# Kernel tuning notes

Hardware: AMD Instinct MI355X
Metric: run time of the kernel (lower is better)

## Reference

```python
import jax, jax.numpy as jnp
import numpy as np

B, T, N, D = 4, 16, 1024, 128
LN_EPS = 1e-5


def setup_inputs() -> dict:
    key = jax.random.key(0)
    k1, k2, k3 = jax.random.split(key, 3)
    X = jax.random.normal(k1, (B, T, N, D), dtype=jnp.float32)
    # normalized adjacency (dense, values in [0,1))
    A = jax.random.uniform(k2, (N, N), dtype=jnp.float32)
    # GCN linear weight (torch nn.Linear, bias=False): out = x @ W.T
    W = jax.random.normal(k3, (D, D), dtype=jnp.float32) / np.sqrt(D)
    gamma = jnp.ones((D,), dtype=jnp.float32)
    beta = jnp.zeros((D,), dtype=jnp.float32)
    return {"X": X, "A": A, "W": W, "gamma": gamma, "beta": beta}


def reference(X, A, W, gamma, beta):
    d = X.shape[-1]
    inv_sqrt_d_a = np.float32(1.0 / np.sqrt(d + 1e-8))  # score scale
    inv_sqrt_d_b = np.float32(1.0 / np.sqrt(d + 1e-9))  # output scale
    # dynamic attention-like scores over nodes: (b,T,N,N)
    scores = jnp.einsum('btnd,btmd->btnm', X, X)
    St = jax.nn.softmax(scores, axis=-1) * inv_sqrt_d_a  # dropout p=0 => identity
    Aeff = A * St                                        # adjacency-masked attention
    # GCN: relu((Aeff @ X) @ W.T)
    h = jnp.einsum('btnm,btmd->btnd', Aeff, X)
    h = jax.nn.relu(h @ W.T) * inv_sqrt_d_b
    # LayerNorm over last dim
    mu = jnp.mean(h, axis=-1, keepdims=True)
    var = jnp.mean(jnp.square(h - mu), axis=-1, keepdims=True)
    h = (h - mu) * jax.lax.rsqrt(var + LN_EPS) * gamma + beta
    # residual
    return h + X
```

## Files before the change

### kernel.cpp

```cpp
#include <hip/hip_runtime.h>


#define NNODES 1024
#define DDIM   128
#define BROWS  128
#define WROWS  16
#define MC     64
#define NCHUNK (NNODES / MC)
#define THREADS 512

#define CA 0.08838834764831845f
#define CB 0.08838834764831845f
#define LN_EPS 1e-5f

typedef __attribute__((ext_vector_type(8))) short bf16x8;
typedef __attribute__((ext_vector_type(4))) float f32x4;

#define XBF_S 136
#define XBT_S 72
#define P_S   72
#define H_S   136
#define XBF_OFF 0
#define XBT_OFF 8704
#define P_OFF   17920
#define SM_TOT  27136

__device__ __forceinline__ unsigned short f2bf(float f) {
  unsigned int u = __float_as_uint(f);
  u += 0x7FFFu + ((u >> 16) & 1u);
  return (unsigned short)(u >> 16);
}

__device__ __forceinline__ bf16x8 pack8(float4 a, float4 b) {
  union { bf16x8 v; unsigned short u[8]; } pk;
  pk.u[0] = f2bf(a.x); pk.u[1] = f2bf(a.y); pk.u[2] = f2bf(a.z); pk.u[3] = f2bf(a.w);
  pk.u[4] = f2bf(b.x); pk.u[5] = f2bf(b.y); pk.u[6] = f2bf(b.z); pk.u[7] = f2bf(b.w);
  return pk.v;
}

__global__ __launch_bounds__(THREADS, 4)
void sdgcn_fused(const float* __restrict__ X, const float* __restrict__ A,
                 const float* __restrict__ W, const float* __restrict__ gamma,
                 const float* __restrict__ beta, float* __restrict__ Out) {
  const int bt   = blockIdx.x;
  const int row0 = blockIdx.y * BROWS;
  const int tid  = (int)threadIdx.x;
  const int wid  = tid >> 6;
  const int lane = tid & 63;
  const int c    = lane & 15;
  const int q    = lane >> 4;

  const float* Xbt = X + (size_t)bt * NNODES * DDIM;

  __shared__ __align__(16) unsigned short sm[SM_TOT];
  unsigned short* Pw = sm + P_OFF + wid * (WROWS * P_S);

  const int wswz = 16 * (q >> 1);
  const int rswz = 16 * ((c >> 3) & 1);

  bf16x8 qfrag[4];
  float cn[4];
  {
    const float* qrow = Xbt + (size_t)(row0 + wid * WROWS + c) * DDIM;
    float ss = 0.f;
#pragma unroll
    for (int ds = 0; ds < 4; ++ds) {
      const float* p = qrow + ds * 32 + q * 8;
      float4 a = *(const float4*)p;
      float4 b = *(const float4*)(p + 4);
      ss += a.x*a.x + a.y*a.y + a.z*a.z + a.w*a.w;
      ss += b.x*b.x + b.y*b.y + b.z*b.z + b.w*b.w;
      qfrag[ds] = pack8(a, b);
    }
    ss += __shfl_xor(ss, 16, 64);
    ss += __shfl_xor(ss, 32, 64);
#pragma unroll
    for (int r = 0; r < 4; ++r)
      cn[r] = __shfl(ss, (lane & 48) + ((lane & 48) >> 2) + r, 64);
  }

  float z_st[4] = {0.f, 0.f, 0.f, 0.f};
  f32x4 Ofr[8];
#pragma unroll
  for (int dt = 0; dt < 8; ++dt) Ofr[dt] = (f32x4){0.f, 0.f, 0.f, 0.f};

  const int grow = row0 + wid * WROWS + q * 4;

  const int sm_ = tid >> 5, sd4 = tid & 31;
  float4 stg[4];
#pragma unroll
  for (int k = 0; k < 4; ++k)
    stg[k] = *(const float4*)(Xbt + (size_t)(sm_ + k * 16) * DDIM + sd4 * 4);

  for (int ch = 0; ch < NCHUNK; ++ch) {
    const int m0 = ch * MC;
#pragma unroll
    for (int k = 0; k < 4; ++k) {
      float4 v = stg[k];
      unsigned int lo = (unsigned int)f2bf(v.x) | ((unsigned int)f2bf(v.y) << 16);
      unsigned int hi = (unsigned int)f2bf(v.z) | ((unsigned int)f2bf(v.w) << 16);
      *(uint2*)(sm + XBF_OFF + (sm_ + k * 16) * XBF_S + sd4 * 4) = make_uint2(lo, hi);
    }
    __syncthreads();
    if (ch + 1 < NCHUNK) {
      const float* nx = Xbt + (size_t)(m0 + MC) * DDIM;
#pragma unroll
      for (int k = 0; k < 4; ++k)
        stg[k] = *(const float4*)(nx + (size_t)(sm_ + k * 16) * DDIM + sd4 * 4);
    }
    float av[4][4];
#pragma unroll
    for (int r = 0; r < 4; ++r)
#pragma unroll
      for (int mt = 0; mt < 4; ++mt)
        av[r][mt] = A[(size_t)(grow + r) * NNODES + m0 + mt*16 + c];
#pragma unroll
    for (int k = 0; k < 2; ++k) {
      int task = tid + k * THREADS;
      int d = task & 127, m8 = task >> 7;
      int base = XBF_OFF + d;
      unsigned int w0 = (unsigned int)sm[base + (m8*8+0)*XBF_S] | ((unsigned int)sm[base + (m8*8+1)*XBF_S] << 16);
      unsigned int w1 = (unsigned int)sm[base + (m8*8+2)*XBF_S] | ((unsigned int)sm[base + (m8*8+3)*XBF_S] << 16);
      unsigned int w2 = (unsigned int)sm[base + (m8*8+4)*XBF_S] | ((unsigned int)sm[base + (m8*8+5)*XBF_S] << 16);
      unsigned int w3 = (unsigned int)sm[base + (m8*8+6)*XBF_S] | ((unsigned int)sm[base + (m8*8+7)*XBF_S] << 16);
      *(uint4*)(sm + XBT_OFF + d * XBT_S + m8 * 8) = make_uint4(w0, w1, w2, w3);
    }
    f32x4 S[4];
#pragma unroll
    for (int mt = 0; mt < 4; ++mt) {
      f32x4 acc = (f32x4){0.f, 0.f, 0.f, 0.f};
#pragma unroll
      for (int ds = 0; ds < 4; ++ds) {
        bf16x8 bf = *(const bf16x8*)(sm + XBF_OFF + (mt*16 + c) * XBF_S + ds*32 + q*8);
        acc = __builtin_amdgcn_mfma_f32_16x16x32_bf16(qfrag[ds], bf, acc, 0, 0, 0);
      }
      S[mt] = acc;
    }
    __syncthreads();
#pragma unroll
    for (int r = 0; r < 4; ++r) {
      float zr = 0.f;
#pragma unroll
      for (int mt = 0; mt < 4; ++mt) {
        float p = __expf(S[mt][r] - cn[r]);
        zr += p;
        Pw[(q*4 + r) * P_S + (((mt*16) ^ wswz) + c)] = f2bf(p * av[r][mt]);
      }
      z_st[r] += zr;
    }
#pragma unroll
    for (int ks = 0; ks < 2; ++ks) {
      bf16x8 pf = *(const bf16x8*)(Pw + c * P_S + (((ks*32 + q*8) ^ rswz)));
#pragma unroll
      for (int dt = 0; dt < 8; ++dt) {
        bf16x8 vf = *(const bf16x8*)(sm + XBT_OFF + (dt*16 + c) * XBT_S + ks*32 + q*8);
        Ofr[dt] = __builtin_amdgcn_mfma_f32_16x16x32_bf16(pf, vf, Ofr[dt], 0, 0, 0);
      }
    }
  }

#pragma unroll
  for (int r = 0; r < 4; ++r) {
    float z = z_st[r];
#pragma unroll
    for (int off = 1; off < 16; off <<= 1) z += __shfl_xor(z, off, 64);
    z_st[r] = z;
  }

  __syncthreads();
  unsigned short* Hw = sm + XBT_OFF + wid * (WROWS * H_S);
#pragma unroll
  for (int r = 0; r < 4; ++r) {
    float rinv = CA / z_st[r];
#pragma unroll
    for (int dt = 0; dt < 8; ++dt)
      Hw[(q*4 + r) * H_S + (((dt*16) ^ wswz) + c)] = f2bf(Ofr[dt][r] * rinv);
  }
  f32x4 G[8];
#pragma unroll
  for (int jt = 0; jt < 8; ++jt) G[jt] = (f32x4){0.f, 0.f, 0.f, 0.f};
#pragma unroll
  for (int ks = 0; ks < 4; ++ks) {
    bf16x8 hf = *(const bf16x8*)(Hw + c * H_S + (((ks*32 + q*8) ^ rswz)));
#pragma unroll
    for (int jt = 0; jt < 8; ++jt) {
      const float* wr = W + (size_t)(jt*16 + c) * DDIM + ks*32 + q*8;
      float4 a = *(const float4*)wr;
      float4 b = *(const float4*)(wr + 4);
      bf16x8 wf = pack8(a, b);
      G[jt] = __builtin_amdgcn_mfma_f32_16x16x32_bf16(hf, wf, G[jt], 0, 0, 0);
    }
  }
#pragma unroll
  for (int jt = 0; jt < 8; ++jt) {
#pragma unroll
    for (int r = 0; r < 4; ++r) G[jt][r] = fmaxf(G[jt][r], 0.f) * CB;
  }
  float* Obt = Out + (size_t)bt * NNODES * DDIM;
#pragma unroll
  for (int r = 0; r < 4; ++r) {
    float s1 = 0.f, s2 = 0.f;
#pragma unroll
    for (int jt = 0; jt < 8; ++jt) { float v = G[jt][r]; s1 += v; s2 += v * v; }
#pragma unroll
    for (int off = 1; off < 16; off <<= 1) {
      s1 += __shfl_xor(s1, off, 64);
      s2 += __shfl_xor(s2, off, 64);
    }
    float mu = s1 * (1.f / 128.f);
    float va = s2 * (1.f / 128.f) - mu * mu;
    float rs = rsqrtf(va + LN_EPS);
    const float* xr = Xbt + (size_t)(grow + r) * DDIM;
    float* orow = Obt + (size_t)(grow + r) * DDIM;
#pragma unroll
    for (int jt = 0; jt < 8; ++jt) {
      int col = jt * 16 + c;
      orow[col] = (G[jt][r] - mu) * rs * gamma[col] + beta[col] + xr[col];
    }
  }
}

extern "C" void kernel_launch(void* const* d_in, const int* in_sizes, int n_in,
                              void* d_out, int out_size, void* d_ws, size_t ws_size,
                              hipStream_t stream) {
  const float* X     = (const float*)d_in[0];
  const float* A     = (const float*)d_in[1];
  const float* W     = (const float*)d_in[2];
  const float* gamma = (const float*)d_in[3];
  const float* beta  = (const float*)d_in[4];
  float* Out = (float*)d_out;
  dim3 grid(64, NNODES / BROWS);
  hipLaunchKernelGGL(sdgcn_fused, grid, dim3(THREADS), 0, stream, X, A, W, gamma, beta, Out);
}
```

Before: 181.4 us.

## Add bf16 prepass that writes X, X-transpose and W to workspace

Adds a prepass kernel that converts X to bf16 in both row-major and transposed layouts, and W to bf16, storing them in the workspace. The main kernel then reads the bf16 keys straight from global/L2 for the score MFMAs, double-buffers the transposed X tiles in shared memory, and loads W already in bf16. This removes the per-chunk fp32-to-bf16 conversion and the LDS transpose that each of the 8 row blocks per batch repeated. In exchange it adds a second launch plus extra workspace writes and reads, and the score B-operand now comes from global memory instead of LDS. The old fused kernel is kept as a fallback when the workspace is too small.

```diff
diff --git a/kernel.cpp b/kernel.cpp
--- a/kernel.cpp
+++ b/kernel.cpp
@@ -3,11 +3,8 @@
 
 #define NNODES 1024
 #define DDIM   128
-#define BROWS  128
-#define WROWS  16
 #define MC     64
 #define NCHUNK (NNODES / MC)
-#define THREADS 512
 
 #define CA 0.08838834764831845f
 #define CB 0.08838834764831845f
@@ -15,6 +12,233 @@
 
 typedef __attribute__((ext_vector_type(8))) short bf16x8;
 typedef __attribute__((ext_vector_type(4))) float f32x4;
+typedef unsigned short ushort_t;
+
+__device__ __forceinline__ unsigned short f2bf(float f) {
+  unsigned int u = __float_as_uint(f);
+  u += 0x7FFFu + ((u >> 16) & 1u);
+  return (unsigned short)(u >> 16);
+}
+__device__ __forceinline__ float bf2f(unsigned short u) {
+  return __uint_as_float(((unsigned int)u) << 16);
+}
+
+__global__ __launch_bounds__(256, 8)
+void sdgcn_prepass(const float* __restrict__ X, const float* __restrict__ W,
+                   ushort_t* __restrict__ Xr, ushort_t* __restrict__ XT,
+                   ushort_t* __restrict__ Wb) {
+  const int bt = blockIdx.x, mt = blockIdx.y, m0 = mt * 64;
+  const int tid = (int)threadIdx.x;
+  __shared__ __align__(16) ushort_t sm[17920];
+  const float* Xs = X + ((size_t)bt * NNODES + m0) * DDIM;
+  ushort_t* Xro = Xr + ((size_t)bt * NNODES + m0) * DDIM;
+#pragma unroll
+  for (int k = 0; k < 8; ++k) {
+    int idx = tid + k * 256;
+    int m = idx >> 5, d4 = idx & 31;
+    float4 v = *(const float4*)(Xs + (size_t)m * DDIM + d4 * 4);
+    unsigned int lo = (unsigned int)f2bf(v.x) | ((unsigned int)f2bf(v.y) << 16);
+    unsigned int hi = (unsigned int)f2bf(v.z) | ((unsigned int)f2bf(v.w) << 16);
+    *(uint2*)(sm + m * 136 + d4 * 4) = make_uint2(lo, hi);
+    *(uint2*)(Xro + (size_t)m * DDIM + d4 * 4) = make_uint2(lo, hi);
+  }
+  __syncthreads();
+#pragma unroll
+  for (int k = 0; k < 4; ++k) {
+    int task = tid + k * 256;
+    int d = task & 127, m8 = task >> 7;
+    int base = d;
+    unsigned int w0 = (unsigned int)sm[base + (m8*8+0)*136] | ((unsigned int)sm[base + (m8*8+1)*136] << 16);
+    unsigned int w1 = (unsigned int)sm[base + (m8*8+2)*136] | ((unsigned int)sm[base + (m8*8+3)*136] << 16);
+    unsigned int w2 = (unsigned int)sm[base + (m8*8+4)*136] | ((unsigned int)sm[base + (m8*8+5)*136] << 16);
+    unsigned int w3 = (unsigned int)sm[base + (m8*8+6)*136] | ((unsigned int)sm[base + (m8*8+7)*136] << 16);
+    *(uint4*)(sm + 8704 + d * 72 + m8 * 8) = make_uint4(w0, w1, w2, w3);
+  }
+  __syncthreads();
+#pragma unroll
+  for (int k = 0; k < 4; ++k) {
+    int task = tid + k * 256;
+    int d = task >> 3, seg = task & 7;
+    uint4 w = *(const uint4*)(sm + 8704 + d * 72 + seg * 8);
+    *(uint4*)(XT + ((size_t)bt * DDIM + d) * NNODES + m0 + seg * 8) = w;
+  }
+  if (bt == 0 && mt < 4) {
+    const float* ws = W + mt * 4096 + tid * 16;
+    ushort_t* wd = Wb + mt * 4096 + tid * 16;
+#pragma unroll
+    for (int k = 0; k < 4; ++k) {
+      float4 v = *(const float4*)(ws + k * 4);
+      unsigned int lo = (unsigned int)f2bf(v.x) | ((unsigned int)f2bf(v.y) << 16);
+      unsigned int hi = (unsigned int)f2bf(v.z) | ((unsigned int)f2bf(v.w) << 16);
+      *(uint2*)(wd + k * 4) = make_uint2(lo, hi);
+    }
+  }
+}
+
+__global__ __launch_bounds__(512, 4)
+void sdgcn_main(const float* __restrict__ X, const float* __restrict__ A,
+                const float* __restrict__ gamma, const float* __restrict__ beta,
+                const ushort_t* __restrict__ Xr, const ushort_t* __restrict__ XT,
+                const ushort_t* __restrict__ Wb, float* __restrict__ Out) {
+  const int bt   = blockIdx.x;
+  const int row0 = blockIdx.y * 128;
+  const int tid  = (int)threadIdx.x;
+  const int wid  = tid >> 6;
+  const int lane = tid & 63;
+  const int c    = lane & 15;
+  const int q    = lane >> 4;
+
+  const ushort_t* Xrb = Xr + (size_t)bt * NNODES * DDIM;
+  const ushort_t* XTb = XT + (size_t)bt * DDIM * NNODES;
+
+  __shared__ __align__(16) ushort_t sm[27648];
+  ushort_t* Pw = sm + 18432 + wid * 1152;
+
+  const int wswz = 16 * (q >> 1);
+  const int rswz = 16 * ((c >> 3) & 1);
+
+  bf16x8 qfrag[4];
+  float cn[4];
+  {
+    const ushort_t* qrow = Xrb + (size_t)(row0 + wid * 16 + c) * DDIM;
+    float ss = 0.f;
+#pragma unroll
+    for (int ds = 0; ds < 4; ++ds) {
+      qfrag[ds] = *(const bf16x8*)(qrow + ds * 32 + q * 8);
+      union { bf16x8 v; unsigned short u[8]; } t; t.v = qfrag[ds];
+#pragma unroll
+      for (int j = 0; j < 8; ++j) { float v = bf2f(t.u[j]); ss += v * v; }
+    }
+    ss += __shfl_xor(ss, 16, 64);
+    ss += __shfl_xor(ss, 32, 64);
+#pragma unroll
+    for (int r = 0; r < 4; ++r)
+      cn[r] = __shfl(ss, (lane & 48) + ((lane & 48) >> 2) + r, 64);
+  }
+
+  float z_st[4] = {0.f, 0.f, 0.f, 0.f};
+  f32x4 Ofr[8];
+#pragma unroll
+  for (int dt = 0; dt < 8; ++dt) Ofr[dt] = (f32x4){0.f, 0.f, 0.f, 0.f};
+
+  const int grow = row0 + wid * 16 + q * 4;
+  const int std_ = tid >> 3, sseg = tid & 7;
+
+#pragma unroll
+  for (int k = 0; k < 2; ++k) {
+    int d = std_ + k * 64, seg = sseg;
+    *(uint4*)(sm + d * 72 + seg * 8) =
+        *(const uint4*)(XTb + (size_t)d * NNODES + seg * 8);
+  }
+
+  for (int ch = 0; ch < NCHUNK; ++ch) {
+    const int m0 = ch * MC;
+    const int cur = (ch & 1) * 9216, nxt = 9216 - cur;
+    __syncthreads();
+    if (ch + 1 < NCHUNK) {
+#pragma unroll
+      for (int k = 0; k < 2; ++k) {
+        int d = std_ + k * 64, seg = sseg;
+        *(uint4*)(sm + nxt + d * 72 + seg * 8) =
+            *(const uint4*)(XTb + (size_t)d * NNODES + (m0 + MC) + seg * 8);
+      }
+    }
+    float av[4][4];
+#pragma unroll
+    for (int r = 0; r < 4; ++r)
+#pragma unroll
+      for (int mt = 0; mt < 4; ++mt)
+        av[r][mt] = A[(size_t)(grow + r) * NNODES + m0 + mt*16 + c];
+    f32x4 S[4];
+#pragma unroll
+    for (int mt = 0; mt < 4; ++mt) {
+      f32x4 acc = (f32x4){0.f, 0.f, 0.f, 0.f};
+#pragma unroll
+      for (int ds = 0; ds < 4; ++ds) {
+        bf16x8 bf = *(const bf16x8*)(Xrb + (size_t)(m0 + mt*16 + c) * DDIM + ds*32 + q*8);
+        acc = __builtin_amdgcn_mfma_f32_16x16x32_bf16(qfrag[ds], bf, acc, 0, 0, 0);
+      }
+      S[mt] = acc;
+    }
+#pragma unroll
+    for (int r = 0; r < 4; ++r) {
+      float zr = 0.f;
+#pragma unroll
+      for (int mt = 0; mt < 4; ++mt) {
+        float p = __expf(S[mt][r] - cn[r]);
+        zr += p;
+        Pw[(q*4 + r) * 72 + (((mt*16) ^ wswz) + c)] = f2bf(p * av[r][mt]);
+      }
+      z_st[r] += zr;
+    }
+#pragma unroll
+    for (int ks = 0; ks < 2; ++ks) {
+      bf16x8 pf = *(const bf16x8*)(Pw + c * 72 + ((ks*32 + q*8) ^ rswz));
+#pragma unroll
+      for (int dt = 0; dt < 8; ++dt) {
+        bf16x8 vf = *(const bf16x8*)(sm + cur + (dt*16 + c) * 72 + ks*32 + q*8);
+        Ofr[dt] = __builtin_amdgcn_mfma_f32_16x16x32_bf16(pf, vf, Ofr[dt], 0, 0, 0);
+      }
+    }
+  }
+
+#pragma unroll
+  for (int r = 0; r < 4; ++r) {
+    float z = z_st[r];
+#pragma unroll
+    for (int off = 1; off < 16; off <<= 1) z += __shfl_xor(z, off, 64);
+    z_st[r] = z;
+  }
+
+  __syncthreads();
+  ushort_t* Hw = sm + wid * 2176;
+#pragma unroll
+  for (int r = 0; r < 4; ++r) {
+    float rinv = CA / z_st[r];
+#pragma unroll
+    for (int dt = 0; dt < 8; ++dt)
+      Hw[(q*4 + r) * 136 + (((dt*16) ^ wswz) + c)] = f2bf(Ofr[dt][r] * rinv);
+  }
+  f32x4 G[8];
+#pragma unroll
+  for (int jt = 0; jt < 8; ++jt) G[jt] = (f32x4){0.f, 0.f, 0.f, 0.f};
+#pragma unroll
+  for (int ks = 0; ks < 4; ++ks) {
+    bf16x8 hf = *(const bf16x8*)(Hw + c * 136 + ((ks*32 + q*8) ^ rswz));
+#pragma unroll
+    for (int jt = 0; jt < 8; ++jt) {
+      bf16x8 wf = *(const bf16x8*)(Wb + (size_t)(jt*16 + c) * DDIM + ks*32 + q*8);
+      G[jt] = __builtin_amdgcn_mfma_f32_16x16x32_bf16(hf, wf, G[jt], 0, 0, 0);
+    }
+  }
+#pragma unroll
+  for (int jt = 0; jt < 8; ++jt)
+#pragma unroll
+    for (int r = 0; r < 4; ++r) G[jt][r] = fmaxf(G[jt][r], 0.f) * CB;
+  const float* Xbt = X + (size_t)bt * NNODES * DDIM;
+  float* Obt = Out + (size_t)bt * NNODES * DDIM;
+#pragma unroll
+  for (int r = 0; r < 4; ++r) {
+    float s1 = 0.f, s2 = 0.f;
+#pragma unroll
+    for (int jt = 0; jt < 8; ++jt) { float v = G[jt][r]; s1 += v; s2 += v * v; }
+#pragma unroll
+    for (int off = 1; off < 16; off <<= 1) {
+      s1 += __shfl_xor(s1, off, 64);
+      s2 += __shfl_xor(s2, off, 64);
+    }
+    float mu = s1 * (1.f / 128.f);
+    float va = s2 * (1.f / 128.f) - mu * mu;
+    float rs = rsqrtf(va + LN_EPS);
+    const float* xr = Xbt + (size_t)(grow + r) * DDIM;
+    float* orow = Obt + (size_t)(grow + r) * DDIM;
+#pragma unroll
+    for (int jt = 0; jt < 8; ++jt) {
+      int col = jt * 16 + c;
+      orow[col] = (G[jt][r] - mu) * rs * gamma[col] + beta[col] + xr[col];
+    }
+  }
+}
 
 #define XBF_S 136
 #define XBT_S 72
@@ -25,12 +249,6 @@
 #define P_OFF   17920
 #define SM_TOT  27136
 
-__device__ __forceinline__ unsigned short f2bf(float f) {
-  unsigned int u = __float_as_uint(f);
-  u += 0x7FFFu + ((u >> 16) & 1u);
-  return (unsigned short)(u >> 16);
-}
-
 __device__ __forceinline__ bf16x8 pack8(float4 a, float4 b) {
   union { bf16x8 v; unsigned short u[8]; } pk;
   pk.u[0] = f2bf(a.x); pk.u[1] = f2bf(a.y); pk.u[2] = f2bf(a.z); pk.u[3] = f2bf(a.w);
@@ -38,30 +256,26 @@
   return pk.v;
 }
 
-__global__ __launch_bounds__(THREADS, 4)
-void sdgcn_fused(const float* __restrict__ X, const float* __restrict__ A,
-                 const float* __restrict__ W, const float* __restrict__ gamma,
-                 const float* __restrict__ beta, float* __restrict__ Out) {
+__global__ __launch_bounds__(512, 4)
+void sdgcn_fallback(const float* __restrict__ X, const float* __restrict__ A,
+                    const float* __restrict__ W, const float* __restrict__ gamma,
+                    const float* __restrict__ beta, float* __restrict__ Out) {
   const int bt   = blockIdx.x;
-  const int row0 = blockIdx.y * BROWS;
+  const int row0 = blockIdx.y * 128;
   const int tid  = (int)threadIdx.x;
   const int wid  = tid >> 6;
   const int lane = tid & 63;
   const int c    = lane & 15;
   const int q    = lane >> 4;
-
   const float* Xbt = X + (size_t)bt * NNODES * DDIM;
-
   __shared__ __align__(16) unsigned short sm[SM_TOT];
-  unsigned short* Pw = sm + P_OFF + wid * (WROWS * P_S);
-
+  unsigned short* Pw = sm + P_OFF + wid * (16 * P_S);
   const int wswz = 16 * (q >> 1);
   const int rswz = 16 * ((c >> 3) & 1);
-
   bf16x8 qfrag[4];
   float cn[4];
   {
-    const float* qrow = Xbt + (size_t)(row0 + wid * WROWS + c) * DDIM;
+    const float* qrow = Xbt + (size_t)(row0 + wid * 16 + c) * DDIM;
     float ss = 0.f;
 #pragma unroll
     for (int ds = 0; ds < 4; ++ds) {
@@ -78,20 +292,16 @@
     for (int r = 0; r < 4; ++r)
       cn[r] = __shfl(ss, (lane & 48) + ((lane & 48) >> 2) + r, 64);
   }
-
   float z_st[4] = {0.f, 0.f, 0.f, 0.f};
   f32x4 Ofr[8];
 #pragma unroll
   for (int dt = 0; dt < 8; ++dt) Ofr[dt] = (f32x4){0.f, 0.f, 0.f, 0.f};
-
-  const int grow = row0 + wid * WROWS + q * 4;
-
+  const int grow = row0 + wid * 16 + q * 4;
   const int sm_ = tid >> 5, sd4 = tid & 31;
   float4 stg[4];
 #pragma unroll
   for (int k = 0; k < 4; ++k)
     stg[k] = *(const float4*)(Xbt + (size_t)(sm_ + k * 16) * DDIM + sd4 * 4);
-
   for (int ch = 0; ch < NCHUNK; ++ch) {
     const int m0 = ch * MC;
 #pragma unroll
@@ -116,7 +326,7 @@
         av[r][mt] = A[(size_t)(grow + r) * NNODES + m0 + mt*16 + c];
 #pragma unroll
     for (int k = 0; k < 2; ++k) {
-      int task = tid + k * THREADS;
+      int task = tid + k * 512;
       int d = task & 127, m8 = task >> 7;
       int base = XBF_OFF + d;
       unsigned int w0 = (unsigned int)sm[base + (m8*8+0)*XBF_S] | ((unsigned int)sm[base + (m8*8+1)*XBF_S] << 16);
@@ -150,7 +360,7 @@
     }
 #pragma unroll
     for (int ks = 0; ks < 2; ++ks) {
-      bf16x8 pf = *(const bf16x8*)(Pw + c * P_S + (((ks*32 + q*8) ^ rswz)));
+      bf16x8 pf = *(const bf16x8*)(Pw + c * P_S + ((ks*32 + q*8) ^ rswz));
 #pragma unroll
       for (int dt = 0; dt < 8; ++dt) {
         bf16x8 vf = *(const bf16x8*)(sm + XBT_OFF + (dt*16 + c) * XBT_S + ks*32 + q*8);
@@ -158,7 +368,6 @@
       }
     }
   }
-
 #pragma unroll
   for (int r = 0; r < 4; ++r) {
     float z = z_st[r];
@@ -166,9 +375,8 @@
     for (int off = 1; off < 16; off <<= 1) z += __shfl_xor(z, off, 64);
     z_st[r] = z;
   }
-
   __syncthreads();
-  unsigned short* Hw = sm + XBT_OFF + wid * (WROWS * H_S);
+  unsigned short* Hw = sm + XBT_OFF + wid * (16 * H_S);
 #pragma unroll
   for (int r = 0; r < 4; ++r) {
     float rinv = CA / z_st[r];
@@ -181,7 +389,7 @@
   for (int jt = 0; jt < 8; ++jt) G[jt] = (f32x4){0.f, 0.f, 0.f, 0.f};
 #pragma unroll
   for (int ks = 0; ks < 4; ++ks) {
-    bf16x8 hf = *(const bf16x8*)(Hw + c * H_S + (((ks*32 + q*8) ^ rswz)));
+    bf16x8 hf = *(const bf16x8*)(Hw + c * H_S + ((ks*32 + q*8) ^ rswz));
 #pragma unroll
     for (int jt = 0; jt < 8; ++jt) {
       const float* wr = W + (size_t)(jt*16 + c) * DDIM + ks*32 + q*8;
@@ -192,10 +400,9 @@
     }
   }
 #pragma unroll
-  for (int jt = 0; jt < 8; ++jt) {
+  for (int jt = 0; jt < 8; ++jt)
 #pragma unroll
     for (int r = 0; r < 4; ++r) G[jt][r] = fmaxf(G[jt][r], 0.f) * CB;
-  }
   float* Obt = Out + (size_t)bt * NNODES * DDIM;
 #pragma unroll
   for (int r = 0; r < 4; ++r) {
@@ -229,6 +436,19 @@
   const float* gamma = (const float*)d_in[3];
   const float* beta  = (const float*)d_in[4];
   float* Out = (float*)d_out;
-  dim3 grid(64, NNODES / BROWS);
-  hipLaunchKernelGGL(sdgcn_fused, grid, dim3(THREADS), 0, stream, X, A, W, gamma, beta, Out);
-}
+
+  const size_t XR_ELEMS = (size_t)64 * NNODES * DDIM;
+  const size_t NEED = (2 * XR_ELEMS + 16384) * sizeof(unsigned short);
+  if (ws_size >= NEED) {
+    ushort_t* Xr = (ushort_t*)d_ws;
+    ushort_t* XT = Xr + XR_ELEMS;
+    ushort_t* Wb = XT + XR_ELEMS;
+    hipLaunchKernelGGL(sdgcn_prepass, dim3(64, 16), dim3(256), 0, stream,
+                       X, W, Xr, XT, Wb);
+    hipLaunchKernelGGL(sdgcn_main, dim3(64, 8), dim3(512), 0, stream,
+                       X, A, gamma, beta, Xr, XT, Wb, Out);
+  } else {
+    hipLaunchKernelGGL(sdgcn_fallback, dim3(64, 8), dim3(512), 0, stream,
+                       X, A, W, gamma, beta, Out);
+  }
+}
```

Result: slower. 253.5 us (+39.7%).

## Switch fused GCN kernel to 32x32x16 MFMA tiles with 4 waves per block

Applied to the files above, without the earlier changes.

Replaces the 16x16x32 bf16 MFMA fragments with 32x32x16 MFMA tiles. Each wave now owns 32 query rows, and the block drops to 256 threads. The softmax shift is folded into the accumulator init as -||x||^2, and gamma/beta loads are hoisted. The aim is fewer MFMA and LDS fragment loads per unit of work, and more reuse per wave. In exchange, each thread holds more registers (16-wide accumulators, larger staging), occupancy is lower, and the LDS swizzles that avoided bank conflicts are dropped.

```diff
diff --git a/kernel.cpp b/kernel.cpp
--- a/kernel.cpp
+++ b/kernel.cpp
@@ -4,17 +4,16 @@
 #define NNODES 1024
 #define DDIM   128
 #define BROWS  128
-#define WROWS  16
 #define MC     64
 #define NCHUNK (NNODES / MC)
-#define THREADS 512
+#define THREADS 256
 
 #define CA 0.08838834764831845f
 #define CB 0.08838834764831845f
 #define LN_EPS 1e-5f
 
-typedef __attribute__((ext_vector_type(8))) short bf16x8;
-typedef __attribute__((ext_vector_type(4))) float f32x4;
+typedef __attribute__((ext_vector_type(8)))  short bf16x8;
+typedef __attribute__((ext_vector_type(16))) float f32x16;
 
 #define XBF_S 136
 #define XBT_S 72
@@ -38,7 +37,7 @@
   return pk.v;
 }
 
-__global__ __launch_bounds__(THREADS, 4)
+__global__ __launch_bounds__(THREADS, 2)
 void sdgcn_fused(const float* __restrict__ X, const float* __restrict__ A,
                  const float* __restrict__ W, const float* __restrict__ gamma,
                  const float* __restrict__ beta, float* __restrict__ Out) {
@@ -47,75 +46,71 @@
   const int tid  = (int)threadIdx.x;
   const int wid  = tid >> 6;
   const int lane = tid & 63;
-  const int c    = lane & 15;
-  const int q    = lane >> 4;
+  const int i32  = lane & 31;
+  const int half = lane >> 5;
 
   const float* Xbt = X + (size_t)bt * NNODES * DDIM;
 
   __shared__ __align__(16) unsigned short sm[SM_TOT];
-  unsigned short* Pw = sm + P_OFF + wid * (WROWS * P_S);
-
-  const int wswz = 16 * (q >> 1);
-  const int rswz = 16 * ((c >> 3) & 1);
-
-  bf16x8 qfrag[4];
-  float cn[4];
+  unsigned short* Pw = sm + P_OFF + wid * 2304;
+
+  const int growb = row0 + wid * 32;
+
+  bf16x8 qfrag[8];
+  float cn[16];
   {
-    const float* qrow = Xbt + (size_t)(row0 + wid * WROWS + c) * DDIM;
+    const float* qrow = Xbt + (size_t)(growb + i32) * DDIM;
     float ss = 0.f;
 #pragma unroll
-    for (int ds = 0; ds < 4; ++ds) {
-      const float* p = qrow + ds * 32 + q * 8;
+    for (int ks = 0; ks < 8; ++ks) {
+      const float* p = qrow + ks * 16 + half * 8;
       float4 a = *(const float4*)p;
       float4 b = *(const float4*)(p + 4);
       ss += a.x*a.x + a.y*a.y + a.z*a.z + a.w*a.w;
       ss += b.x*b.x + b.y*b.y + b.z*b.z + b.w*b.w;
-      qfrag[ds] = pack8(a, b);
-    }
-    ss += __shfl_xor(ss, 16, 64);
+      qfrag[ks] = pack8(a, b);
+    }
     ss += __shfl_xor(ss, 32, 64);
 #pragma unroll
-    for (int r = 0; r < 4; ++r)
-      cn[r] = __shfl(ss, (lane & 48) + ((lane & 48) >> 2) + r, 64);
-  }
-
-  float z_st[4] = {0.f, 0.f, 0.f, 0.f};
-  f32x4 Ofr[8];
-#pragma unroll
-  for (int dt = 0; dt < 8; ++dt) Ofr[dt] = (f32x4){0.f, 0.f, 0.f, 0.f};
-
-  const int grow = row0 + wid * WROWS + q * 4;
-
-  const int sm_ = tid >> 5, sd4 = tid & 31;
-  float4 stg[4];
-#pragma unroll
-  for (int k = 0; k < 4; ++k)
-    stg[k] = *(const float4*)(Xbt + (size_t)(sm_ + k * 16) * DDIM + sd4 * 4);
+    for (int r = 0; r < 16; ++r) {
+      int rr = (r & 3) + 8 * (r >> 2) + 4 * half;
+      cn[r] = __shfl(ss, rr, 64);
+    }
+  }
+
+  float z_st[16];
+#pragma unroll
+  for (int r = 0; r < 16; ++r) z_st[r] = 0.f;
+  f32x16 Ofr[4];
+#pragma unroll
+  for (int dt = 0; dt < 4; ++dt)
+#pragma unroll
+    for (int r = 0; r < 16; ++r) Ofr[dt][r] = 0.f;
+
+  const int smr = tid >> 5, sd4 = tid & 31;
+  float4 stg[8];
+#pragma unroll
+  for (int k = 0; k < 8; ++k)
+    stg[k] = *(const float4*)(Xbt + (size_t)(smr + 8*k) * DDIM + sd4 * 4);
 
   for (int ch = 0; ch < NCHUNK; ++ch) {
     const int m0 = ch * MC;
 #pragma unroll
-    for (int k = 0; k < 4; ++k) {
+    for (int k = 0; k < 8; ++k) {
       float4 v = stg[k];
       unsigned int lo = (unsigned int)f2bf(v.x) | ((unsigned int)f2bf(v.y) << 16);
       unsigned int hi = (unsigned int)f2bf(v.z) | ((unsigned int)f2bf(v.w) << 16);
-      *(uint2*)(sm + XBF_OFF + (sm_ + k * 16) * XBF_S + sd4 * 4) = make_uint2(lo, hi);
+      *(uint2*)(sm + XBF_OFF + (smr + 8*k) * XBF_S + sd4 * 4) = make_uint2(lo, hi);
     }
     __syncthreads();
     if (ch + 1 < NCHUNK) {
       const float* nx = Xbt + (size_t)(m0 + MC) * DDIM;
 #pragma unroll
-      for (int k = 0; k < 4; ++k)
-        stg[k] = *(const float4*)(nx + (size_t)(sm_ + k * 16) * DDIM + sd4 * 4);
-    }
-    float av[4][4];
-#pragma unroll
-    for (int r = 0; r < 4; ++r)
-#pragma unroll
-      for (int mt = 0; mt < 4; ++mt)
-        av[r][mt] = A[(size_t)(grow + r) * NNODES + m0 + mt*16 + c];
-#pragma unroll
-    for (int k = 0; k < 2; ++k) {
+      for (int k = 0; k < 8; ++k)
+        stg[k] = *(const float4*)(nx + (size_t)(smr + 8*k) * DDIM + sd4 * 4);
+    }
+#pragma unroll
+    for (int k = 0; k < 4; ++k) {
       int task = tid + k * THREADS;
       int d = task & 127, m8 = task >> 7;
       int base = XBF_OFF + d;
@@ -125,97 +120,115 @@
       unsigned int w3 = (unsigned int)sm[base + (m8*8+6)*XBF_S] | ((unsigned int)sm[base + (m8*8+7)*XBF_S] << 16);
       *(uint4*)(sm + XBT_OFF + d * XBT_S + m8 * 8) = make_uint4(w0, w1, w2, w3);
     }
-    f32x4 S[4];
-#pragma unroll
-    for (int mt = 0; mt < 4; ++mt) {
-      f32x4 acc = (f32x4){0.f, 0.f, 0.f, 0.f};
-#pragma unroll
-      for (int ds = 0; ds < 4; ++ds) {
-        bf16x8 bf = *(const bf16x8*)(sm + XBF_OFF + (mt*16 + c) * XBF_S + ds*32 + q*8);
-        acc = __builtin_amdgcn_mfma_f32_16x16x32_bf16(qfrag[ds], bf, acc, 0, 0, 0);
+    f32x16 S[2];
+#pragma unroll
+    for (int mt = 0; mt < 2; ++mt) {
+      f32x16 acc;
+#pragma unroll
+      for (int r = 0; r < 16; ++r) acc[r] = -cn[r];
+#pragma unroll
+      for (int ks = 0; ks < 8; ++ks) {
+        bf16x8 bf = *(const bf16x8*)(sm + XBF_OFF + (mt*32 + i32) * XBF_S + ks*16 + half*8);
+        acc = __builtin_amdgcn_mfma_f32_32x32x16_bf16(qfrag[ks], bf, acc, 0, 0, 0);
       }
       S[mt] = acc;
     }
     __syncthreads();
-#pragma unroll
-    for (int r = 0; r < 4; ++r) {
-      float zr = 0.f;
-#pragma unroll
-      for (int mt = 0; mt < 4; ++mt) {
-        float p = __expf(S[mt][r] - cn[r]);
-        zr += p;
-        Pw[(q*4 + r) * P_S + (((mt*16) ^ wswz) + c)] = f2bf(p * av[r][mt]);
+    float av[16][2];
+#pragma unroll
+    for (int r = 0; r < 16; ++r) {
+      int rr = (r & 3) + 8 * (r >> 2) + 4 * half;
+#pragma unroll
+      for (int mt = 0; mt < 2; ++mt)
+        av[r][mt] = A[(size_t)(growb + rr) * NNODES + m0 + mt*32 + i32];
+    }
+#pragma unroll
+    for (int r = 0; r < 16; ++r) {
+      int rr = (r & 3) + 8 * (r >> 2) + 4 * half;
+#pragma unroll
+      for (int mt = 0; mt < 2; ++mt) {
+        float p = __expf(S[mt][r]);
+        z_st[r] += p;
+        Pw[rr * P_S + mt*32 + i32] = f2bf(p * av[r][mt]);
       }
-      z_st[r] += zr;
-    }
-#pragma unroll
-    for (int ks = 0; ks < 2; ++ks) {
-      bf16x8 pf = *(const bf16x8*)(Pw + c * P_S + (((ks*32 + q*8) ^ rswz)));
-#pragma unroll
-      for (int dt = 0; dt < 8; ++dt) {
-        bf16x8 vf = *(const bf16x8*)(sm + XBT_OFF + (dt*16 + c) * XBT_S + ks*32 + q*8);
-        Ofr[dt] = __builtin_amdgcn_mfma_f32_16x16x32_bf16(pf, vf, Ofr[dt], 0, 0, 0);
+    }
+#pragma unroll
+    for (int ks = 0; ks < 4; ++ks) {
+      bf16x8 pf = *(const bf16x8*)(Pw + i32 * P_S + ks*16 + half*8);
+#pragma unroll
+      for (int dt = 0; dt < 4; ++dt) {
+        bf16x8 vf = *(const bf16x8*)(sm + XBT_OFF + (dt*32 + i32) * XBT_S + ks*16 + half*8);
+        Ofr[dt] = __builtin_amdgcn_mfma_f32_32x32x16_bf16(pf, vf, Ofr[dt], 0, 0, 0);
       }
     }
   }
 
 #pragma unroll
-  for (int r = 0; r < 4; ++r) {
+  for (int r = 0; r < 16; ++r) {
     float z = z_st[r];
 #pragma unroll
-    for (int off = 1; off < 16; off <<= 1) z += __shfl_xor(z, off, 64);
+    for (int off = 1; off < 32; off <<= 1) z += __shfl_xor(z, off, 64);
     z_st[r] = z;
   }
 
   __syncthreads();
-  unsigned short* Hw = sm + XBT_OFF + wid * (WROWS * H_S);
-#pragma unroll
-  for (int r = 0; r < 4; ++r) {
+  unsigned short* Hw = sm + wid * (32 * H_S);
+#pragma unroll
+  for (int r = 0; r < 16; ++r) {
+    int rr = (r & 3) + 8 * (r >> 2) + 4 * half;
     float rinv = CA / z_st[r];
 #pragma unroll
-    for (int dt = 0; dt < 8; ++dt)
-      Hw[(q*4 + r) * H_S + (((dt*16) ^ wswz) + c)] = f2bf(Ofr[dt][r] * rinv);
-  }
-  f32x4 G[8];
-#pragma unroll
-  for (int jt = 0; jt < 8; ++jt) G[jt] = (f32x4){0.f, 0.f, 0.f, 0.f};
-#pragma unroll
-  for (int ks = 0; ks < 4; ++ks) {
-    bf16x8 hf = *(const bf16x8*)(Hw + c * H_S + (((ks*32 + q*8) ^ rswz)));
-#pragma unroll
-    for (int jt = 0; jt < 8; ++jt) {
-      const float* wr = W + (size_t)(jt*16 + c) * DDIM + ks*32 + q*8;
+    for (int dt = 0; dt < 4; ++dt)
+      Hw[rr * H_S + dt*32 + i32] = f2bf(Ofr[dt][r] * rinv);
+  }
+  f32x16 G[4];
+#pragma unroll
+  for (int jt = 0; jt < 4; ++jt)
+#pragma unroll
+    for (int r = 0; r < 16; ++r) G[jt][r] = 0.f;
+#pragma unroll
+  for (int ks = 0; ks < 8; ++ks) {
+    bf16x8 hf = *(const bf16x8*)(Hw + i32 * H_S + ks*16 + half*8);
+#pragma unroll
+    for (int jt = 0; jt < 4; ++jt) {
+      const float* wr = W + (size_t)(jt*32 + i32) * DDIM + ks*16 + half*8;
       float4 a = *(const float4*)wr;
       float4 b = *(const float4*)(wr + 4);
       bf16x8 wf = pack8(a, b);
-      G[jt] = __builtin_amdgcn_mfma_f32_16x16x32_bf16(hf, wf, G[jt], 0, 0, 0);
-    }
-  }
-#pragma unroll
-  for (int jt = 0; jt < 8; ++jt) {
-#pragma unroll
-    for (int r = 0; r < 4; ++r) G[jt][r] = fmaxf(G[jt][r], 0.f) * CB;
+      G[jt] = __builtin_amdgcn_mfma_f32_32x32x16_bf16(hf, wf, G[jt], 0, 0, 0);
+    }
+  }
+#pragma unroll
+  for (int jt = 0; jt < 4; ++jt)
+#pragma unroll
+    for (int r = 0; r < 16; ++r) G[jt][r] = fmaxf(G[jt][r], 0.f) * CB;
+  float gj[4], bj[4];
+#pragma unroll
+  for (int jt = 0; jt < 4; ++jt) {
+    gj[jt] = gamma[jt*32 + i32];
+    bj[jt] = beta[jt*32 + i32];
   }
   float* Obt = Out + (size_t)bt * NNODES * DDIM;
 #pragma unroll
-  for (int r = 0; r < 4; ++r) {
+  for (int r = 0; r < 16; ++r) {
+    int rr = (r & 3) + 8 * (r >> 2) + 4 * half;
     float s1 = 0.f, s2 = 0.f;
 #pragma unroll
-    for (int jt = 0; jt < 8; ++jt) { float v = G[jt][r]; s1 += v; s2 += v * v; }
-#pragma unroll
-    for (int off = 1; off < 16; off <<= 1) {
+    for (int jt = 0; jt < 4; ++jt) { float v = G[jt][r]; s1 += v; s2 += v * v; }
+#pragma unroll
+    for (int off = 1; off < 32; off <<= 1) {
       s1 += __shfl_xor(s1, off, 64);
       s2 += __shfl_xor(s2, off, 64);
     }
     float mu = s1 * (1.f / 128.f);
     float va = s2 * (1.f / 128.f) - mu * mu;
     float rs = rsqrtf(va + LN_EPS);
-    const float* xr = Xbt + (size_t)(grow + r) * DDIM;
-    float* orow = Obt + (size_t)(grow + r) * DDIM;
-#pragma unroll
-    for (int jt = 0; jt < 8; ++jt) {
-      int col = jt * 16 + c;
-      orow[col] = (G[jt][r] - mu) * rs * gamma[col] + beta[col] + xr[col];
+    const float* xr = Xbt + (size_t)(growb + rr) * DDIM;
+    float* orow = Obt + (size_t)(growb + rr) * DDIM;
+#pragma unroll
+    for (int jt = 0; jt < 4; ++jt) {
+      int col = jt * 32 + i32;
+      orow[col] = (G[jt][r] - mu) * rs * gj[jt] + bj[jt] + xr[col];
     }
   }
 }
```

Measured after the change: 215.9 us. 19.0% more time.
